# Performance work log

Hardware: AMD Instinct MI355X
Metric: run time of the kernel (lower is better)

## Reference

```python
import jax, jax.numpy as jnp
import numpy as np

EPS = 1e-5

def _ln(x, w, b):
    mu = x.mean(-1, keepdims=True)
    var = ((x - mu) ** 2).mean(-1, keepdims=True)
    return (x - mu) * jax.lax.rsqrt(var + EPS) * w + b

def _shift(x):
    # ZeroPad2d((0,0,1,-1)): x_shifted[:, t] = x[:, t-1], zero at t=0
    return jnp.pad(x, ((0, 0), (1, 0), (0, 0)))[:, :-1]

def _time_mix(x, u, w, mk, mv, mr, Wk, Wv, Wr, Wo, bo):
    xs = _shift(x)
    k = (x * mk + xs * (1 - mk)) @ Wk.T            # [B,T,d]
    v = (x * mv + xs * (1 - mv)) @ Wv.T
    r = jax.nn.sigmoid(x * mr + xs * (1 - mr)) @ Wr.T
    B, T, d = x.shape

    def step(carry, kv):
        a, b = carry
        kt, vt = kv                                 # [B,d]
        q = jnp.maximum(u + kt, w)
        e1 = jnp.exp(-w - q)
        e2 = jnp.exp(u + kt - q)
        a = e1 * a + e2 * vt
        b = e1 * b + e2
        return (a, b), a / b

    a0 = jnp.zeros((B, d), x.dtype)
    b0 = jnp.zeros((B, d), x.dtype)
    _, wkv = jax.lax.scan(step, (a0, b0), (k.transpose(1, 0, 2), v.transpose(1, 0, 2)))
    wkv = wkv.transpose(1, 0, 2)                    # [B,T,d]
    return (wkv * r) @ Wo.T + bo

def _channel_mix(x, mk, mr, Wk, Wv, Wr):
    xs = _shift(x)
    k = jnp.square(jax.nn.relu((x * mk + xs * (1 - mk)) @ Wk.T))
    v = k @ Wv.T
    r = jax.nn.sigmoid((x * mr + xs * (1 - mr)) @ Wr.T)
    return r * v

def setup_inputs() -> dict:
    B, T, d = 8, 2048, 2048
    key = jax.random.key(0)
    ks = jax.random.split(key, 16)
    s = 0.02
    return {
        "x": jax.random.normal(ks[0], (B, T, d), jnp.float32),
        "ln1_w": jnp.ones((d,), jnp.float32),
        "ln1_b": jnp.zeros((d,), jnp.float32),
        "ln2_w": jnp.ones((d,), jnp.float32),
        "ln2_b": jnp.zeros((d,), jnp.float32),
        "tm_u": 0.1 * jax.random.normal(ks[1], (d,), jnp.float32),
        "tm_w": jnp.ones((d,), jnp.float32) + 0.1 * jax.random.normal(ks[2], (d,), jnp.float32),
        "tm_mix_k": jax.random.uniform(ks[3], (d,), jnp.float32),
        "tm_mix_v": jax.random.uniform(ks[4], (d,), jnp.float32),
        "tm_mix_r": jax.random.uniform(ks[5], (d,), jnp.float32),
        "tm_Wk": s * jax.random.normal(ks[6], (d, d), jnp.float32),
        "tm_Wv": s * jax.random.normal(ks[7], (d, d), jnp.float32),
        "tm_Wr": s * jax.random.normal(ks[8], (d, d), jnp.float32),
        "tm_Wo": s * jax.random.normal(ks[9], (d, d), jnp.float32),
        "tm_bo": jnp.zeros((d,), jnp.float32),
        "cm_mix_k": jax.random.uniform(ks[10], (d,), jnp.float32),
        "cm_mix_r": jax.random.uniform(ks[11], (d,), jnp.float32),
        "cm_Wk": s * jax.random.normal(ks[12], (d, d), jnp.float32),
        "cm_Wv": s * jax.random.normal(ks[13], (d, d), jnp.float32),
        "cm_Wr": s * jax.random.normal(ks[14], (d, d), jnp.float32),
    }

def reference(x, ln1_w, ln1_b, ln2_w, ln2_b, tm_u, tm_w, tm_mix_k, tm_mix_v, tm_mix_r, tm_Wk, tm_Wv, tm_Wr, tm_Wo, tm_bo, cm_mix_k, cm_mix_r, cm_Wk, cm_Wv, cm_Wr):
    att = _time_mix(_ln(x, ln1_w, ln1_b), tm_u, tm_w, tm_mix_k, tm_mix_v, tm_mix_r, tm_Wk, tm_Wv, tm_Wr, tm_Wo, tm_bo)
    x = x + att
    ffn = _channel_mix(_ln(x, ln2_w, ln2_b), cm_mix_k, cm_mix_r, cm_Wk, cm_Wv, cm_Wr)
    return x + ffn
```

## Files before the change

### kernel.cpp

```cpp
#include <hip/hip_runtime.h>
#include <hip/hip_bf16.h>
#include <stdint.h>

typedef __bf16 bf16x8 __attribute__((ext_vector_type(8)));
typedef float floatx4 __attribute__((ext_vector_type(4)));

__device__ __forceinline__ float bf2f(__hip_bfloat16 v) { return __bfloat162float(v); }
__device__ __forceinline__ __hip_bfloat16 f2bf(float v) { return __float2bfloat16(v); }

#define WKV_CH 64

__global__ __launch_bounds__(256) void k_f2bf(const float* __restrict__ in,
                                              __hip_bfloat16* __restrict__ out, int n) {
    int i = blockIdx.x * 256 + threadIdx.x;
    if (i < n) out[i] = f2bf(in[i]);
}

__global__ __launch_bounds__(256) void k_ln(const float* __restrict__ x,
                                            const float* __restrict__ w,
                                            const float* __restrict__ b,
                                            __hip_bfloat16* __restrict__ out, int d) {
    __shared__ float red[8];
    const size_t row = blockIdx.x;
    const float* xr = x + row * (size_t)d;
    float s = 0.f, ss = 0.f;
    for (int i = threadIdx.x; i < d; i += 256) {
        float v = xr[i];
        s += v; ss += v * v;
    }
    for (int off = 32; off > 0; off >>= 1) {
        s  += __shfl_down(s,  off, 64);
        ss += __shfl_down(ss, off, 64);
    }
    int wv = threadIdx.x >> 6, ln = threadIdx.x & 63;
    if (ln == 0) { red[wv] = s; red[4 + wv] = ss; }
    __syncthreads();
    s  = red[0] + red[1] + red[2] + red[3];
    ss = red[4] + red[5] + red[6] + red[7];
    float mu  = s / d;
    float var = ss / d - mu * mu;
    float rs  = rsqrtf(var + 1e-5f);
    __hip_bfloat16* orow = out + row * (size_t)d;
    for (int i = threadIdx.x; i < d; i += 256) {
        orow[i] = f2bf((xr[i] - mu) * rs * w[i] + b[i]);
    }
}

__global__ __launch_bounds__(256) void k_tmix(const __hip_bfloat16* __restrict__ xln,
    const float* __restrict__ mk, const float* __restrict__ mv, const float* __restrict__ mr,
    __hip_bfloat16* __restrict__ xk, __hip_bfloat16* __restrict__ xv, __hip_bfloat16* __restrict__ xr,
    int T, int d) {
    const int c = blockIdx.x * 256 + threadIdx.x;
    const size_t row = blockIdx.y;
    const int t = (int)(row % (size_t)T);
    const size_t idx = row * (size_t)d + c;
    float xc = bf2f(xln[idx]);
    float xs = t ? bf2f(xln[idx - d]) : 0.f;
    float a = mk[c];
    xk[idx] = f2bf(xc * a + xs * (1.f - a));
    float bq = mv[c];
    xv[idx] = f2bf(xc * bq + xs * (1.f - bq));
    float rm = mr[c];
    float pre = xc * rm + xs * (1.f - rm);
    xr[idx] = f2bf(1.f / (1.f + __expf(-pre)));
}

__global__ __launch_bounds__(256) void k_cmix(const __hip_bfloat16* __restrict__ xln,
    const float* __restrict__ mk, const float* __restrict__ mr,
    __hip_bfloat16* __restrict__ xk, __hip_bfloat16* __restrict__ xr,
    int T, int d) {
    const int c = blockIdx.x * 256 + threadIdx.x;
    const size_t row = blockIdx.y;
    const int t = (int)(row % (size_t)T);
    const size_t idx = row * (size_t)d + c;
    float xc = bf2f(xln[idx]);
    float xs = t ? bf2f(xln[idx - d]) : 0.f;
    float a = mk[c];
    xk[idx] = f2bf(xc * a + xs * (1.f - a));
    float rm = mr[c];
    xr[idx] = f2bf(xc * rm + xs * (1.f - rm));
}

__global__ __launch_bounds__(256) void k_wkv_p1(const __hip_bfloat16* __restrict__ k,
    const __hip_bfloat16* __restrict__ v,
    const float* __restrict__ u, const float* __restrict__ w,
    float* __restrict__ Ac, float* __restrict__ Bc, float* __restrict__ Pc,
    int T, int d, int nch) {
    const int idx = blockIdx.x * 256 + threadIdx.x;
    const int c = idx & (d - 1);
    const int rest = idx / d;
    const int j = rest & (nch - 1);
    const int b = rest / nch;
    const float uc = u[c], wc = w[c];
    float aa = 0.f, bb = 0.f, P = 0.f;
    const size_t base = ((size_t)b * T + (size_t)j * WKV_CH) * d + c;
#pragma unroll 4
    for (int t = 0; t < WKV_CH; ++t) {
        float kt = bf2f(k[base + (size_t)t * d]);
        float vt = bf2f(v[base + (size_t)t * d]);
        float q  = fmaxf(uc + kt, wc);
        float e1 = __expf(-wc - q);
        float e2 = __expf(uc + kt - q);
        aa = e1 * aa + e2 * vt;
        bb = e1 * bb + e2;
        P += wc + q;
    }
    const size_t s = ((size_t)b * nch + j) * d + c;
    Ac[s] = aa; Bc[s] = bb; Pc[s] = P;
}

__global__ __launch_bounds__(256) void k_wkv_p2(const float* __restrict__ Ac,
    const float* __restrict__ Bc, const float* __restrict__ Pc,
    float* __restrict__ Ain, float* __restrict__ Bin, int d, int nch) {
    const int idx = blockIdx.x * 256 + threadIdx.x;
    const int c = idx & (d - 1);
    const int b = idx / d;
    float a = 0.f, bbs = 0.f;
    for (int j = 0; j < nch; ++j) {
        const size_t s = ((size_t)b * nch + j) * d + c;
        Ain[s] = a; Bin[s] = bbs;
        float p = __expf(-Pc[s]);
        a   = p * a   + Ac[s];
        bbs = p * bbs + Bc[s];
    }
}

__global__ __launch_bounds__(256) void k_wkv_p3(const __hip_bfloat16* __restrict__ k,
    const __hip_bfloat16* v,
    const __hip_bfloat16* __restrict__ r,
    const float* __restrict__ u, const float* __restrict__ w,
    const float* __restrict__ Ain, const float* __restrict__ Bin,
    __hip_bfloat16* out, int T, int d, int nch) {
    const int idx = blockIdx.x * 256 + threadIdx.x;
    const int c = idx & (d - 1);
    const int rest = idx / d;
    const int j = rest & (nch - 1);
    const int b = rest / nch;
    const float uc = u[c], wc = w[c];
    const size_t s = ((size_t)b * nch + j) * d + c;
    float aa = Ain[s], bb = Bin[s];
    const size_t base = ((size_t)b * T + (size_t)j * WKV_CH) * d + c;
#pragma unroll 4
    for (int t = 0; t < WKV_CH; ++t) {
        float kt = bf2f(k[base + (size_t)t * d]);
        float vt = bf2f(v[base + (size_t)t * d]);
        float rt = bf2f(r[base + (size_t)t * d]);
        float q  = fmaxf(uc + kt, wc);
        float e1 = __expf(-wc - q);
        float e2 = __expf(uc + kt - q);
        aa = e1 * aa + e2 * vt;
        bb = e1 * bb + e2;
        out[base + (size_t)t * d] = f2bf((aa / bb) * rt);
    }
}

#define GM_BF16  0
#define GM_ADDX  1
#define GM_SIG   2
#define GM_RELU2 3
#define GM_FINAL 4

template<int MODE>
__global__ __launch_bounds__(256, 2)
void gemm_bt(const __hip_bfloat16* __restrict__ A,
             const __hip_bfloat16* __restrict__ B,
             void* __restrict__ outv,
             const float* __restrict__ auxf,
             const float* __restrict__ bias,
             const __hip_bfloat16* __restrict__ auxb,
             int N, int K) {
    __shared__ unsigned short As[128 * 32];
    __shared__ unsigned short Bs[128 * 32];
    const int tid  = threadIdx.x;
    const int lane = tid & 63;
    const int wave = tid >> 6;
    const int waveM = (wave >> 1) << 6;
    const int waveN = (wave & 1) << 6;
    const int bm = blockIdx.y * 128;
    const int bn = blockIdx.x * 128;

    const int srow = lane >> 2;
    const int scol = (lane & 3) << 3;
    const __hip_bfloat16* Ag = A + (size_t)(bm + wave * 32 + srow) * K + scol;
    const __hip_bfloat16* Bg = B + (size_t)(bn + wave * 32 + srow) * K + scol;
    unsigned short* As0 = As + wave * 1024;
    unsigned short* Bs0 = Bs + wave * 1024;

    floatx4 acc[4][4] = {};
    const int aoff = ((lane & 15) * 32) + ((lane >> 4) << 3);

    for (int k0 = 0; k0 < K; k0 += 32) {
        __builtin_amdgcn_global_load_lds(
            (__attribute__((address_space(1))) void*)(Ag + k0),
            (__attribute__((address_space(3))) void*)(As0), 16, 0, 0);
        __builtin_amdgcn_global_load_lds(
            (__attribute__((address_space(1))) void*)(Ag + k0 + (size_t)16 * K),
            (__attribute__((address_space(3))) void*)(As0 + 512), 16, 0, 0);
        __builtin_amdgcn_global_load_lds(
            (__attribute__((address_space(1))) void*)(Bg + k0),
            (__attribute__((address_space(3))) void*)(Bs0), 16, 0, 0);
        __builtin_amdgcn_global_load_lds(
            (__attribute__((address_space(1))) void*)(Bg + k0 + (size_t)16 * K),
            (__attribute__((address_space(3))) void*)(Bs0 + 512), 16, 0, 0);
        __syncthreads();
        bf16x8 af[4], bfr[4];
#pragma unroll
        for (int i = 0; i < 4; ++i) {
            af[i]  = *reinterpret_cast<const bf16x8*>(As + (waveM + i * 16) * 32 + aoff);
            bfr[i] = *reinterpret_cast<const bf16x8*>(Bs + (waveN + i * 16) * 32 + aoff);
        }
#pragma unroll
        for (int mt = 0; mt < 4; ++mt)
#pragma unroll
            for (int nt = 0; nt < 4; ++nt)
                acc[mt][nt] = __builtin_amdgcn_mfma_f32_16x16x32_bf16(af[mt], bfr[nt], acc[mt][nt], 0, 0, 0);
        __syncthreads();
    }

    const int colb = bn + waveN + (lane & 15);
    const int rowb = bm + waveM + ((lane >> 4) << 2);
#pragma unroll
    for (int mt = 0; mt < 4; ++mt) {
#pragma unroll
        for (int nt = 0; nt < 4; ++nt) {
            const int c = colb + nt * 16;
#pragma unroll
            for (int j = 0; j < 4; ++j) {
                const int row = rowb + mt * 16 + j;
                const size_t idx = (size_t)row * N + c;
                const float val = acc[mt][nt][j];
                if (MODE == GM_BF16) {
                    ((__hip_bfloat16*)outv)[idx] = f2bf(val);
                } else if (MODE == GM_ADDX) {
                    ((float*)outv)[idx] = auxf[idx] + bias[c] + val;
                } else if (MODE == GM_SIG) {
                    ((__hip_bfloat16*)outv)[idx] = f2bf(1.f / (1.f + __expf(-val)));
                } else if (MODE == GM_RELU2) {
                    float tpos = fmaxf(val, 0.f);
                    ((__hip_bfloat16*)outv)[idx] = f2bf(tpos * tpos);
                } else {
                    float* o = (float*)outv;
                    o[idx] = o[idx] + bf2f(auxb[idx]) * val;
                }
            }
        }
    }
}

extern "C" void kernel_launch(void* const* d_in, const int* in_sizes, int n_in,
                              void* d_out, int out_size, void* d_ws, size_t ws_size,
                              hipStream_t stream) {
    const float* x      = (const float*)d_in[0];
    const float* ln1_w  = (const float*)d_in[1];
    const float* ln1_b  = (const float*)d_in[2];
    const float* ln2_w  = (const float*)d_in[3];
    const float* ln2_b  = (const float*)d_in[4];
    const float* tm_u   = (const float*)d_in[5];
    const float* tm_w   = (const float*)d_in[6];
    const float* tm_mk  = (const float*)d_in[7];
    const float* tm_mv  = (const float*)d_in[8];
    const float* tm_mr  = (const float*)d_in[9];
    const float* tm_bo  = (const float*)d_in[14];
    const float* cm_mk  = (const float*)d_in[15];
    const float* cm_mr  = (const float*)d_in[16];

    const int D = in_sizes[1];
    const int Mrows = in_sizes[0] / D;
    const int T = 2048;
    const int Bb = Mrows / T;
    const size_t dd = (size_t)D * D;
    const size_t md = (size_t)Mrows * D;
    const int nch = T / WKV_CH;

    __hip_bfloat16* W = (__hip_bfloat16*)d_ws;
    __hip_bfloat16* buf[7];
    for (int i = 0; i < 7; ++i) buf[i] = W + 7 * dd + (size_t)i * md;

    float* S = (float*)buf[0];
    const size_t cs = (size_t)Bb * nch * D;
    float* Ac  = S;
    float* Bc  = S + cs;
    float* Pc  = S + 2 * cs;
    float* Ain = S + 3 * cs;
    float* Bin = S + 4 * cs;

    const int widx[7] = {10, 11, 12, 13, 17, 18, 19};
    for (int i = 0; i < 7; ++i)
        k_f2bf<<<(int)(dd / 256), 256, 0, stream>>>((const float*)d_in[widx[i]], W + (size_t)i * dd, (int)dd);

    k_ln<<<Mrows, 256, 0, stream>>>(x, ln1_w, ln1_b, buf[0], D);
    k_tmix<<<dim3(D / 256, Mrows), 256, 0, stream>>>(buf[0], tm_mk, tm_mv, tm_mr,
                                                     buf[1], buf[2], buf[3], T, D);
    dim3 gg(D / 128, Mrows / 128);
    gemm_bt<GM_BF16><<<gg, 256, 0, stream>>>(buf[1], W + 0 * dd, buf[4], nullptr, nullptr, nullptr, D, D);
    gemm_bt<GM_BF16><<<gg, 256, 0, stream>>>(buf[2], W + 1 * dd, buf[5], nullptr, nullptr, nullptr, D, D);
    gemm_bt<GM_BF16><<<gg, 256, 0, stream>>>(buf[3], W + 2 * dd, buf[6], nullptr, nullptr, nullptr, D, D);

    k_wkv_p1<<<(Bb * D * nch) / 256, 256, 0, stream>>>(buf[4], buf[5], tm_u, tm_w,
                                                       Ac, Bc, Pc, T, D, nch);
    k_wkv_p2<<<(Bb * D) / 256, 256, 0, stream>>>(Ac, Bc, Pc, Ain, Bin, D, nch);
    k_wkv_p3<<<(Bb * D * nch) / 256, 256, 0, stream>>>(buf[4], buf[5], buf[6], tm_u, tm_w,
                                                       Ain, Bin, buf[5], T, D, nch);

    gemm_bt<GM_ADDX><<<gg, 256, 0, stream>>>(buf[5], W + 3 * dd, d_out, x, tm_bo, nullptr, D, D);
    k_ln<<<Mrows, 256, 0, stream>>>((const float*)d_out, ln2_w, ln2_b, buf[0], D);
    k_cmix<<<dim3(D / 256, Mrows), 256, 0, stream>>>(buf[0], cm_mk, cm_mr, buf[1], buf[2], T, D);
    gemm_bt<GM_SIG><<<gg, 256, 0, stream>>>(buf[2], W + 6 * dd, buf[3], nullptr, nullptr, nullptr, D, D);
    gemm_bt<GM_RELU2><<<gg, 256, 0, stream>>>(buf[1], W + 4 * dd, buf[6], nullptr, nullptr, nullptr, D, D);
    gemm_bt<GM_FINAL><<<gg, 256, 0, stream>>>(buf[6], W + 5 * dd, d_out, nullptr, nullptr, buf[3], D, D);
}
```

Measured before the change: 1.956 ms.

## Rewrite GEMM as 256x256 double-buffered pipelined kernel with swizzled LDS

After: 1.736 ms. 11.2% less time.

```diff
diff --git a/kernel.cpp b/kernel.cpp
--- a/kernel.cpp
+++ b/kernel.cpp
@@ -160,8 +160,11 @@
 #define GM_RELU2 3
 #define GM_FINAL 4
 
+#define REGLDS(reg) ((unsigned)((reg) == 0 ? 0u : (reg) == 1 ? 32768u : (reg) == 2 ? 16384u : 49152u))
+#define SBAR() __builtin_amdgcn_sched_barrier(0)
+
 template<int MODE>
-__global__ __launch_bounds__(256, 2)
+__global__ __launch_bounds__(512, 2)
 void gemm_bt(const __hip_bfloat16* __restrict__ A,
              const __hip_bfloat16* __restrict__ B,
              void* __restrict__ outv,
@@ -169,82 +172,175 @@
              const float* __restrict__ bias,
              const __hip_bfloat16* __restrict__ auxb,
              int N, int K) {
-    __shared__ unsigned short As[128 * 32];
-    __shared__ unsigned short Bs[128 * 32];
+    __shared__ char smem[131072];
     const int tid  = threadIdx.x;
     const int lane = tid & 63;
     const int wave = tid >> 6;
-    const int waveM = (wave >> 1) << 6;
-    const int waveN = (wave & 1) << 6;
-    const int bm = blockIdx.y * 128;
-    const int bn = blockIdx.x * 128;
-
-    const int srow = lane >> 2;
-    const int scol = (lane & 3) << 3;
-    const __hip_bfloat16* Ag = A + (size_t)(bm + wave * 32 + srow) * K + scol;
-    const __hip_bfloat16* Bg = B + (size_t)(bn + wave * 32 + srow) * K + scol;
-    unsigned short* As0 = As + wave * 1024;
-    unsigned short* Bs0 = Bs + wave * 1024;
-
-    floatx4 acc[4][4] = {};
-    const int aoff = ((lane & 15) * 32) + ((lane >> 4) << 3);
-
-    for (int k0 = 0; k0 < K; k0 += 32) {
-        __builtin_amdgcn_global_load_lds(
-            (__attribute__((address_space(1))) void*)(Ag + k0),
-            (__attribute__((address_space(3))) void*)(As0), 16, 0, 0);
-        __builtin_amdgcn_global_load_lds(
-            (__attribute__((address_space(1))) void*)(Ag + k0 + (size_t)16 * K),
-            (__attribute__((address_space(3))) void*)(As0 + 512), 16, 0, 0);
-        __builtin_amdgcn_global_load_lds(
-            (__attribute__((address_space(1))) void*)(Bg + k0),
-            (__attribute__((address_space(3))) void*)(Bs0), 16, 0, 0);
-        __builtin_amdgcn_global_load_lds(
-            (__attribute__((address_space(1))) void*)(Bg + k0 + (size_t)16 * K),
-            (__attribute__((address_space(3))) void*)(Bs0 + 512), 16, 0, 0);
-        __syncthreads();
-        bf16x8 af[4], bfr[4];
+    const int wm = wave >> 2;
+    const int wn = wave & 3;
+    const int NT = K >> 6;
+    const size_t Kb = (size_t)K * 2;
+
+    const int bn = blockIdx.x * 256;
+    const int bm = blockIdx.y * 256;
+
+    const int rh0 = tid >> 3;
+    const int kc8 = ((tid & 7) ^ (rh0 & 7)) << 3;
+    const size_t offA = ((size_t)(bm + rh0) * K + kc8) * 2;
+    const size_t offB = ((size_t)(bn + rh0) * K + kc8) * 2;
+    const unsigned waveBase = (unsigned)(wave * 64);
+
+#define STAGE(tau, reg) do {                                                        \
+    int _tt = (tau);                                                                \
+    if (_tt < NT) {                                                                 \
+        const char* _gp = ((reg) & 1) ? (const char*)B : (const char*)A;            \
+        size_t _go = (((reg) & 1) ? offB : offA)                                    \
+                   + (((reg) >= 2) ? (size_t)128 * Kb : 0) + (size_t)_tt * 128;     \
+        unsigned _lb = ((unsigned)(_tt & 1) << 16) + REGLDS(reg);                   \
+        _Pragma("unroll")                                                           \
+        for (int _q = 0; _q < 2; ++_q) {                                            \
+            __builtin_amdgcn_global_load_lds(                                       \
+                (__attribute__((address_space(1))) void*)(_gp + _go + (size_t)_q * 64 * Kb), \
+                (__attribute__((address_space(3))) void*)(smem + _lb + (unsigned)(_q * 512 + waveBase) * 16), \
+                16, 0, 0);                                                          \
+        }                                                                           \
+    }                                                                               \
+} while (0)
+
+    const int lane15 = lane & 15;
+    const int laneHi = lane >> 4;
+    const int chunk0 = ((laneHi)     ^ (lane & 7)) << 4;
+    const int chunk1 = ((laneHi + 4) ^ (lane & 7)) << 4;
+    const int aLane = (wm * 64 + lane15) * 128;
+    const int bLane = 32768 + (wn * 32 + lane15) * 128;
+
+    floatx4 acc00[4][2] = {}, acc01[4][2] = {}, acc11[4][2] = {}, acc10[4][2] = {};
+    bf16x8 a[4][2], b0[2][2], b1[2][2];
+
+    STAGE(0, 0); STAGE(0, 1); STAGE(0, 2); STAGE(0, 3);
+    STAGE(1, 0); STAGE(1, 1); STAGE(1, 2);
+    asm volatile("s_waitcnt vmcnt(6)" ::: "memory");
+    SBAR(); __builtin_amdgcn_s_barrier(); SBAR();
+
+#pragma unroll 2
+    for (int t = 0; t < NT; ++t) {
+        const char* sA = smem + ((t & 1) << 16) + aLane;
+        const char* sB = smem + ((t & 1) << 16) + bLane;
+
 #pragma unroll
         for (int i = 0; i < 4; ++i) {
-            af[i]  = *reinterpret_cast<const bf16x8*>(As + (waveM + i * 16) * 32 + aoff);
-            bfr[i] = *reinterpret_cast<const bf16x8*>(Bs + (waveN + i * 16) * 32 + aoff);
+            a[i][0] = *(const bf16x8*)(sA + i * 2048 + chunk0);
+            a[i][1] = *(const bf16x8*)(sA + i * 2048 + chunk1);
         }
 #pragma unroll
-        for (int mt = 0; mt < 4; ++mt)
-#pragma unroll
-            for (int nt = 0; nt < 4; ++nt)
-                acc[mt][nt] = __builtin_amdgcn_mfma_f32_16x16x32_bf16(af[mt], bfr[nt], acc[mt][nt], 0, 0, 0);
-        __syncthreads();
-    }
-
-    const int colb = bn + waveN + (lane & 15);
-    const int rowb = bm + waveM + ((lane >> 4) << 2);
-#pragma unroll
-    for (int mt = 0; mt < 4; ++mt) {
-#pragma unroll
-        for (int nt = 0; nt < 4; ++nt) {
-            const int c = colb + nt * 16;
-#pragma unroll
-            for (int j = 0; j < 4; ++j) {
-                const int row = rowb + mt * 16 + j;
-                const size_t idx = (size_t)row * N + c;
-                const float val = acc[mt][nt][j];
-                if (MODE == GM_BF16) {
-                    ((__hip_bfloat16*)outv)[idx] = f2bf(val);
-                } else if (MODE == GM_ADDX) {
-                    ((float*)outv)[idx] = auxf[idx] + bias[c] + val;
-                } else if (MODE == GM_SIG) {
-                    ((__hip_bfloat16*)outv)[idx] = f2bf(1.f / (1.f + __expf(-val)));
-                } else if (MODE == GM_RELU2) {
-                    float tpos = fmaxf(val, 0.f);
-                    ((__hip_bfloat16*)outv)[idx] = f2bf(tpos * tpos);
-                } else {
-                    float* o = (float*)outv;
-                    o[idx] = o[idx] + bf2f(auxb[idx]) * val;
-                }
+        for (int j = 0; j < 2; ++j) {
+            b0[j][0] = *(const bf16x8*)(sB + j * 2048 + chunk0);
+            b0[j][1] = *(const bf16x8*)(sB + j * 2048 + chunk1);
+        }
+        STAGE(t + 1, 3);
+        SBAR(); __builtin_amdgcn_s_barrier(); SBAR();
+        __builtin_amdgcn_s_setprio(1);
+#pragma unroll
+        for (int i = 0; i < 4; ++i)
+#pragma unroll
+            for (int j = 0; j < 2; ++j) {
+                acc00[i][j] = __builtin_amdgcn_mfma_f32_16x16x32_bf16(a[i][0], b0[j][0], acc00[i][j], 0, 0, 0);
+                acc00[i][j] = __builtin_amdgcn_mfma_f32_16x16x32_bf16(a[i][1], b0[j][1], acc00[i][j], 0, 0, 0);
             }
+        __builtin_amdgcn_s_setprio(0);
+        SBAR(); __builtin_amdgcn_s_barrier(); SBAR();
+
+#pragma unroll
+        for (int j = 0; j < 2; ++j) {
+            b1[j][0] = *(const bf16x8*)(sB + 16384 + j * 2048 + chunk0);
+            b1[j][1] = *(const bf16x8*)(sB + 16384 + j * 2048 + chunk1);
         }
-    }
+        STAGE(t + 2, 0);
+        SBAR(); __builtin_amdgcn_s_barrier(); SBAR();
+        __builtin_amdgcn_s_setprio(1);
+#pragma unroll
+        for (int i = 0; i < 4; ++i)
+#pragma unroll
+            for (int j = 0; j < 2; ++j) {
+                acc01[i][j] = __builtin_amdgcn_mfma_f32_16x16x32_bf16(a[i][0], b1[j][0], acc01[i][j], 0, 0, 0);
+                acc01[i][j] = __builtin_amdgcn_mfma_f32_16x16x32_bf16(a[i][1], b1[j][1], acc01[i][j], 0, 0, 0);
+            }
+        __builtin_amdgcn_s_setprio(0);
+        SBAR(); __builtin_amdgcn_s_barrier(); SBAR();
+
+#pragma unroll
+        for (int i = 0; i < 4; ++i) {
+            a[i][0] = *(const bf16x8*)(sA + 16384 + i * 2048 + chunk0);
+            a[i][1] = *(const bf16x8*)(sA + 16384 + i * 2048 + chunk1);
+        }
+        STAGE(t + 2, 1);
+        SBAR(); __builtin_amdgcn_s_barrier(); SBAR();
+        __builtin_amdgcn_s_setprio(1);
+#pragma unroll
+        for (int i = 0; i < 4; ++i)
+#pragma unroll
+            for (int j = 0; j < 2; ++j) {
+                acc11[i][j] = __builtin_amdgcn_mfma_f32_16x16x32_bf16(a[i][0], b1[j][0], acc11[i][j], 0, 0, 0);
+                acc11[i][j] = __builtin_amdgcn_mfma_f32_16x16x32_bf16(a[i][1], b1[j][1], acc11[i][j], 0, 0, 0);
+            }
+        __builtin_amdgcn_s_setprio(0);
+        SBAR(); __builtin_amdgcn_s_barrier(); SBAR();
+
+        STAGE(t + 2, 2);
+        SBAR(); __builtin_amdgcn_s_barrier(); SBAR();
+        __builtin_amdgcn_s_setprio(1);
+#pragma unroll
+        for (int i = 0; i < 4; ++i)
+#pragma unroll
+            for (int j = 0; j < 2; ++j) {
+                acc10[i][j] = __builtin_amdgcn_mfma_f32_16x16x32_bf16(a[i][0], b0[j][0], acc10[i][j], 0, 0, 0);
+                acc10[i][j] = __builtin_amdgcn_mfma_f32_16x16x32_bf16(a[i][1], b0[j][1], acc10[i][j], 0, 0, 0);
+            }
+        __builtin_amdgcn_s_setprio(0);
+        SBAR();
+        if (t + 2 < NT) {
+            asm volatile("s_waitcnt vmcnt(6)" ::: "memory");
+        } else {
+            asm volatile("s_waitcnt vmcnt(0)" ::: "memory");
+        }
+        __builtin_amdgcn_s_barrier(); SBAR();
+    }
+#undef STAGE
+
+    const int erow = bm + wm * 64 + (laneHi << 2);
+    const int ecol = bn + wn * 32 + lane15;
+#define EPI(ACC, MH, NH)                                                            \
+    _Pragma("unroll")                                                               \
+    for (int i = 0; i < 4; ++i) {                                                   \
+        _Pragma("unroll")                                                           \
+        for (int jf = 0; jf < 2; ++jf) {                                            \
+            const int c = ecol + (NH) * 128 + jf * 16;                              \
+            _Pragma("unroll")                                                       \
+            for (int j = 0; j < 4; ++j) {                                           \
+                const int r = erow + (MH) * 128 + i * 16 + j;                       \
+                const size_t idx = (size_t)r * N + c;                               \
+                const float val = ACC[i][jf][j];                                    \
+                if (MODE == GM_BF16) {                                              \
+                    ((__hip_bfloat16*)outv)[idx] = f2bf(val);                       \
+                } else if (MODE == GM_ADDX) {                                       \
+                    ((float*)outv)[idx] = auxf[idx] + bias[c] + val;                \
+                } else if (MODE == GM_SIG) {                                        \
+                    ((__hip_bfloat16*)outv)[idx] = f2bf(1.f / (1.f + __expf(-val))); \
+                } else if (MODE == GM_RELU2) {                                      \
+                    float tp = fmaxf(val, 0.f);                                     \
+                    ((__hip_bfloat16*)outv)[idx] = f2bf(tp * tp);                   \
+                } else {                                                            \
+                    float* o = (float*)outv;                                        \
+                    o[idx] = o[idx] + bf2f(auxb[idx]) * val;                        \
+                }                                                                   \
+            }                                                                       \
+        }                                                                           \
+    }
+    EPI(acc00, 0, 0)
+    EPI(acc01, 0, 1)
+    EPI(acc11, 1, 1)
+    EPI(acc10, 1, 0)
+#undef EPI
 }
 
 extern "C" void kernel_launch(void* const* d_in, const int* in_sizes, int n_in,
@@ -291,10 +387,10 @@
     k_ln<<<Mrows, 256, 0, stream>>>(x, ln1_w, ln1_b, buf[0], D);
     k_tmix<<<dim3(D / 256, Mrows), 256, 0, stream>>>(buf[0], tm_mk, tm_mv, tm_mr,
                                                      buf[1], buf[2], buf[3], T, D);
-    dim3 gg(D / 128, Mrows / 128);
-    gemm_bt<GM_BF16><<<gg, 256, 0, stream>>>(buf[1], W + 0 * dd, buf[4], nullptr, nullptr, nullptr, D, D);
-    gemm_bt<GM_BF16><<<gg, 256, 0, stream>>>(buf[2], W + 1 * dd, buf[5], nullptr, nullptr, nullptr, D, D);
-    gemm_bt<GM_BF16><<<gg, 256, 0, stream>>>(buf[3], W + 2 * dd, buf[6], nullptr, nullptr, nullptr, D, D);
+    dim3 gg(D / 256, Mrows / 256);
+    gemm_bt<GM_BF16><<<gg, 512, 0, stream>>>(buf[1], W + 0 * dd, buf[4], nullptr, nullptr, nullptr, D, D);
+    gemm_bt<GM_BF16><<<gg, 512, 0, stream>>>(buf[2], W + 1 * dd, buf[5], nullptr, nullptr, nullptr, D, D);
+    gemm_bt<GM_BF16><<<gg, 512, 0, stream>>>(buf[3], W + 2 * dd, buf[6], nullptr, nullptr, nullptr, D, D);
 
     k_wkv_p1<<<(Bb * D * nch) / 256, 256, 0, stream>>>(buf[4], buf[5], tm_u, tm_w,
                                                        Ac, Bc, Pc, T, D, nch);
@@ -302,10 +398,10 @@
     k_wkv_p3<<<(Bb * D * nch) / 256, 256, 0, stream>>>(buf[4], buf[5], buf[6], tm_u, tm_w,
                                                        Ain, Bin, buf[5], T, D, nch);
 
-    gemm_bt<GM_ADDX><<<gg, 256, 0, stream>>>(buf[5], W + 3 * dd, d_out, x, tm_bo, nullptr, D, D);
+    gemm_bt<GM_ADDX><<<gg, 512, 0, stream>>>(buf[5], W + 3 * dd, d_out, x, tm_bo, nullptr, D, D);
     k_ln<<<Mrows, 256, 0, stream>>>((const float*)d_out, ln2_w, ln2_b, buf[0], D);
     k_cmix<<<dim3(D / 256, Mrows), 256, 0, stream>>>(buf[0], cm_mk, cm_mr, buf[1], buf[2], T, D);
-    gemm_bt<GM_SIG><<<gg, 256, 0, stream>>>(buf[2], W + 6 * dd, buf[3], nullptr, nullptr, nullptr, D, D);
-    gemm_bt<GM_RELU2><<<gg, 256, 0, stream>>>(buf[1], W + 4 * dd, buf[6], nullptr, nullptr, nullptr, D, D);
-    gemm_bt<GM_FINAL><<<gg, 256, 0, stream>>>(buf[6], W + 5 * dd, d_out, nullptr, nullptr, buf[3], D, D);
-}
+    gemm_bt<GM_SIG><<<gg, 512, 0, stream>>>(buf[2], W + 6 * dd, buf[3], nullptr, nullptr, nullptr, D, D);
+    gemm_bt<GM_RELU2><<<gg, 512, 0, stream>>>(buf[1], W + 4 * dd, buf[6], nullptr, nullptr, nullptr, D, D);
+    gemm_bt<GM_FINAL><<<gg, 512, 0, stream>>>(buf[6], W + 5 * dd, d_out, nullptr, nullptr, buf[3], D, D);
+}
```
